# Optimization experiments

Measured on AMD Instinct MI355X. Metric: run time of the kernel, lower is better.

The kernel has to match this reference:

```python
import jax, jax.numpy as jnp
import numpy as np

NUM_HEADS = 8
WINDOW = 5
DILATION = 1


def _offsets(window, dilation):
    r = dilation * (window // 2)
    return [(dy, dx) for dy in range(-r, r + 1, dilation)
            for dx in range(-r, r + 1, dilation)]


def _neighbors(x, window, dilation):
    # x: [B, heads, head_dim, Hc, Wc] -> [B, heads, K, head_dim, Hc, Wc]
    B, Hn, hd, Hc, Wc = x.shape
    r = dilation * (window // 2)
    xp = jnp.pad(x, ((0, 0), (0, 0), (0, 0), (r, r), (r, r)))
    offs = _offsets(window, dilation)
    return jnp.stack(
        [xp[..., r + dy:r + dy + Hc, r + dx:r + dx + Wc] for dy, dx in offs],
        axis=2)


def _valid_mask(Hc, Wc, window, dilation):
    # [K, Hc, Wc] bool: True where the shifted neighbor lies inside the map
    ys = jnp.arange(Hc)
    xs = jnp.arange(Wc)
    offs = _offsets(window, dilation)
    return jnp.stack(
        [(((ys + dy) >= 0) & ((ys + dy) < Hc))[:, None]
         & (((xs + dx) >= 0) & ((xs + dx) < Wc))[None, :]
         for dy, dx in offs], axis=0)


def _align_to_query_grid(t, out_h, out_w, scale):
    # repeat coarse lattice onto the fine query grid via anchor indexing
    y = jnp.clip(jnp.arange(out_h) // scale, 0, t.shape[-2] - 1)
    x = jnp.clip(jnp.arange(out_w) // scale, 0, t.shape[-1] - 1)
    return jnp.take(jnp.take(t, y, axis=-2), x, axis=-1)


def setup_inputs() -> dict:
    key = jax.random.key(0)
    k1, k2 = jax.random.split(key)
    k = jax.random.normal(k1, (2, 128, 48, 48), dtype=jnp.float32)
    v = jax.random.normal(k2, (2, 128, 48, 48), dtype=jnp.float32)
    return {"k": k, "v": v, "query_height": 96, "query_width": 96,
            "scale_factor": 2}


def reference(k, v, query_height, query_width, scale_factor):
    B, C, Hc, Wc = k.shape
    hd = C // NUM_HEADS
    kh = k.reshape(B, NUM_HEADS, hd, Hc, Wc)
    vh = v.reshape(B, NUM_HEADS, hd, Hc, Wc)
    k_nb = _neighbors(kh, WINDOW, DILATION)  # [B,H,K,hd,Hc,Wc]
    v_nb = _neighbors(vh, WINDOW, DILATION)
    mask = _valid_mask(Hc, Wc, WINDOW, DILATION)  # [K,Hc,Wc]
    K = mask.shape[0]
    mask = jnp.broadcast_to(mask[None, None], (B, NUM_HEADS, K, Hc, Wc))
    k_nb = _align_to_query_grid(k_nb, query_height, query_width, scale_factor)
    v_nb = _align_to_query_grid(v_nb, query_height, query_width, scale_factor)
    mask = _align_to_query_grid(mask, query_height, query_width, scale_factor)
    return (k_nb, v_nb, mask)
```

## Files before the change

kernel.cpp:

```cpp
#include <hip/hip_runtime.h>


#define HC 48
#define WC 48

__global__ __launch_bounds__(384) void fused_expand(
    const float* __restrict__ k, const float* __restrict__ v,
    float* __restrict__ out_k, float* __restrict__ out_v,
    float* __restrict__ out_m) {
    int t  = blockIdx.x * 384 + threadIdx.x;
    int yc = t / 24;
    int x4 = t - yc * 24;
    int by = blockIdx.y;

    if (by < 6400) {
        int d    = by & 15;
        int rest = by >> 4;
        int kk   = rest % 25;
        int bh   = rest / 25;
        int dy = kk / 5 - 2;
        int dx = kk % 5 - 2;

        int yy  = yc + dy;
        bool vy = (unsigned)yy < (unsigned)HC;
        int xc0 = 2 * x4 + dx;
        int xc1 = xc0 + 1;
        bool m0 = vy && ((unsigned)xc0 < (unsigned)WC);
        bool m1 = vy && ((unsigned)xc1 < (unsigned)WC);

        int src = ((bh * 16 + d) * HC + (vy ? yy : 0)) * WC;
        float k0 = m0 ? k[src + xc0] : 0.0f;
        float k1 = m1 ? k[src + xc1] : 0.0f;
        float w0 = m0 ? v[src + xc0] : 0.0f;
        float w1 = m1 ? v[src + xc1] : 0.0f;

        float4 ok = make_float4(k0, k0, k1, k1);
        float4 ov = make_float4(w0, w0, w1, w1);
        int o = by * 2304 + yc * 48 + x4;
        float4* pk = reinterpret_cast<float4*>(out_k);
        float4* pv = reinterpret_cast<float4*>(out_v);
        pk[o]      = ok;
        pk[o + 24] = ok;
        pv[o]      = ov;
        pv[o + 24] = ov;
    } else {
        int q  = by - 6400;
        int kk = q % 25;
        int dy = kk / 5 - 2;
        int dx = kk % 5 - 2;

        int yy  = yc + dy;
        bool vy = (unsigned)yy < (unsigned)HC;
        int xc0 = 2 * x4 + dx;
        bool m0 = vy && ((unsigned)xc0 < (unsigned)WC);
        bool m1 = vy && ((unsigned)(xc0 + 1) < (unsigned)WC);

        float f0 = m0 ? 1.0f : 0.0f;
        float f1 = m1 ? 1.0f : 0.0f;
        float4 m = make_float4(f0, f0, f1, f1);
        int o = q * 2304 + yc * 48 + x4;
        float4* pm = reinterpret_cast<float4*>(out_m);
        pm[o]      = m;
        pm[o + 24] = m;
    }
}

extern "C" void kernel_launch(void* const* d_in, const int* in_sizes, int n_in,
                              void* d_out, int out_size, void* d_ws, size_t ws_size,
                              hipStream_t stream) {
    const float* k = (const float*)d_in[0];
    const float* v = (const float*)d_in[1];
    float* out   = (float*)d_out;
    float* out_k = out;
    float* out_v = out + 58982400;
    float* out_m = out + 117964800;

    dim3 grid(3, 6800, 1);
    fused_expand<<<grid, 384, 0, stream>>>(k, v, out_k, out_v, out_m);
}
```

Before: 486.6 us.

## Stage input tiles in shared memory and emit all 25 offsets per block

Each block now loads a half-channel tile of k and v (with a zero-padded halo) into shared memory once. It then loops over all 25 window offsets and writes every expanded output from LDS, so the repeated global gathers and boundary predicates go away. Mask blocks now write all 16 batch-head copies from one computed value. The grid shrinks from 20400 blocks to 562 larger blocks, which lowers parallelism and could hurt occupancy, since the kernel is bound by output writes.

```diff
diff --git a/kernel.cpp b/kernel.cpp
--- a/kernel.cpp
+++ b/kernel.cpp
@@ -1,67 +1,94 @@
 #include <hip/hip_runtime.h>
 
 
-#define HC 48
-#define WC 48
+#define ROWS 28
+#define RSTRIDE 56
+#define C0 4
 
-__global__ __launch_bounds__(384) void fused_expand(
+__global__ __launch_bounds__(576) void expand_kernel(
     const float* __restrict__ k, const float* __restrict__ v,
     float* __restrict__ out_k, float* __restrict__ out_v,
     float* __restrict__ out_m) {
-    int t  = blockIdx.x * 384 + threadIdx.x;
-    int yc = t / 24;
-    int x4 = t - yc * 24;
-    int by = blockIdx.y;
+    int bid = blockIdx.x;
+    int tid = threadIdx.x;
+    int ycl = tid / 24;
+    int x4  = tid - ycl * 24;
 
-    if (by < 6400) {
-        int d    = by & 15;
-        int rest = by >> 4;
-        int kk   = rest % 25;
-        int bh   = rest / 25;
+    if (bid < 512) {
+        __shared__ float smem[2][ROWS * RSTRIDE];
+
+        int ch = bid >> 1;
+        int s  = bid & 1;
+        int bh = ch >> 4;
+        int d  = ch & 15;
+        int yc0 = 24 * s;
+
+        float4* z = reinterpret_cast<float4*>(&smem[0][0]);
+        for (int i = tid; i < 2 * ROWS * RSTRIDE / 4; i += 576)
+            z[i] = make_float4(0.f, 0.f, 0.f, 0.f);
+        __syncthreads();
+
+        const float4* gk = reinterpret_cast<const float4*>(k) + ch * 576;
+        const float4* gv = reinterpret_cast<const float4*>(v) + ch * 576;
+        for (int i = tid; i < 2 * ROWS * 12; i += 576) {
+            int which = i >= ROWS * 12;
+            int j = i - which * ROWS * 12;
+            int r = j / 12, c = j - r * 12;
+            int g = yc0 - 2 + r;
+            if ((unsigned)g < 48u) {
+                float4 val = which ? gv[g * 12 + c] : gk[g * 12 + c];
+                float4* dst = reinterpret_cast<float4*>(
+                    &smem[which][r * RSTRIDE + C0 + 4 * c]);
+                *dst = val;
+            }
+        }
+        __syncthreads();
+
+        int yc = yc0 + ycl;
+        const float* sk = &smem[0][(ycl + 2) * RSTRIDE + C0 + 2 * x4];
+        const float* sv = &smem[1][(ycl + 2) * RSTRIDE + C0 + 2 * x4];
+        long long o = (long long)(bh * 25 * 16 + d) * 2304 + yc * 48 + x4;
+        float4* pk = reinterpret_cast<float4*>(out_k);
+        float4* pv = reinterpret_cast<float4*>(out_v);
+
+        for (int dy = -2; dy <= 2; ++dy) {
+#pragma unroll
+            for (int dx = -2; dx <= 2; ++dx) {
+                int ld = dy * RSTRIDE + dx;
+                float k0 = sk[ld], k1 = sk[ld + 1];
+                float w0 = sv[ld], w1 = sv[ld + 1];
+                float4 ok = make_float4(k0, k0, k1, k1);
+                float4 ov = make_float4(w0, w0, w1, w1);
+                pk[o]      = ok;
+                pk[o + 24] = ok;
+                pv[o]      = ov;
+                pv[o + 24] = ov;
+                o += 16 * 2304;
+            }
+        }
+    } else {
+        int mb = bid - 512;
+        int kk = mb >> 1;
+        int s  = mb & 1;
         int dy = kk / 5 - 2;
         int dx = kk % 5 - 2;
+        int yc = s * 24 + ycl;
 
-        int yy  = yc + dy;
-        bool vy = (unsigned)yy < (unsigned)HC;
+        int yy = yc + dy;
+        bool vy = (unsigned)yy < 48u;
         int xc0 = 2 * x4 + dx;
-        int xc1 = xc0 + 1;
-        bool m0 = vy && ((unsigned)xc0 < (unsigned)WC);
-        bool m1 = vy && ((unsigned)xc1 < (unsigned)WC);
+        float m0 = (vy && (unsigned)xc0 < 48u) ? 1.0f : 0.0f;
+        float m1 = (vy && (unsigned)(xc0 + 1) < 48u) ? 1.0f : 0.0f;
+        float4 m = make_float4(m0, m0, m1, m1);
 
-        int src = ((bh * 16 + d) * HC + (vy ? yy : 0)) * WC;
-        float k0 = m0 ? k[src + xc0] : 0.0f;
-        float k1 = m1 ? k[src + xc1] : 0.0f;
-        float w0 = m0 ? v[src + xc0] : 0.0f;
-        float w1 = m1 ? v[src + xc1] : 0.0f;
-
-        float4 ok = make_float4(k0, k0, k1, k1);
-        float4 ov = make_float4(w0, w0, w1, w1);
-        int o = by * 2304 + yc * 48 + x4;
-        float4* pk = reinterpret_cast<float4*>(out_k);
-        float4* pv = reinterpret_cast<float4*>(out_v);
-        pk[o]      = ok;
-        pk[o + 24] = ok;
-        pv[o]      = ov;
-        pv[o + 24] = ov;
-    } else {
-        int q  = by - 6400;
-        int kk = q % 25;
-        int dy = kk / 5 - 2;
-        int dx = kk % 5 - 2;
-
-        int yy  = yc + dy;
-        bool vy = (unsigned)yy < (unsigned)HC;
-        int xc0 = 2 * x4 + dx;
-        bool m0 = vy && ((unsigned)xc0 < (unsigned)WC);
-        bool m1 = vy && ((unsigned)(xc0 + 1) < (unsigned)WC);
-
-        float f0 = m0 ? 1.0f : 0.0f;
-        float f1 = m1 ? 1.0f : 0.0f;
-        float4 m = make_float4(f0, f0, f1, f1);
-        int o = q * 2304 + yc * 48 + x4;
         float4* pm = reinterpret_cast<float4*>(out_m);
-        pm[o]      = m;
-        pm[o + 24] = m;
+        long long o = (long long)kk * 2304 + yc * 48 + x4;
+#pragma unroll
+        for (int bh = 0; bh < 16; ++bh) {
+            pm[o]      = m;
+            pm[o + 24] = m;
+            o += 57600;
+        }
     }
 }
 
@@ -75,6 +102,5 @@
     float* out_v = out + 58982400;
     float* out_m = out + 117964800;
 
-    dim3 grid(3, 6800, 1);
-    fused_expand<<<grid, 384, 0, stream>>>(k, v, out_k, out_v, out_m);
+    expand_kernel<<<562, 576, 0, stream>>>(k, v, out_k, out_v, out_m);
 }
```

Result: no change. 482.8 us (-0.8%).
